# Optimization experiments

Hardware: AMD Instinct MI355X
Metric: run time of the kernel (lower is better)

## Reference

```python
import jax, jax.numpy as jnp
import numpy as np
import math

NUM_HEADS = 4


def setup_inputs() -> dict:
    key = jax.random.key(0)
    k1, k2, k3, k4 = jax.random.split(key, 4)
    b, c, f, t = 8, 512, 32, 64
    x = jax.random.normal(k1, (b, c, f, t), dtype=jnp.float32)
    # Conv1d(k=1) weights stored as 2D (out, in); fan-in scaled like torch default
    qkv_w = jax.random.normal(k2, (3 * c, c), dtype=jnp.float32) / math.sqrt(c)
    qkv_b = jax.random.normal(k3, (3 * c,), dtype=jnp.float32) * 0.02
    proj_w = jax.random.normal(k4, (c, c), dtype=jnp.float32) / math.sqrt(c)
    proj_b = jnp.zeros((c,), dtype=jnp.float32)
    return {"x": x, "qkv_w": qkv_w, "qkv_b": qkv_b, "proj_w": proj_w, "proj_b": proj_b}


def reference(x, qkv_w, qkv_b, proj_w, proj_b):
    b, c, f, t = x.shape
    T = f * t
    xr = x.reshape(b, c, T)  # [b, c, T]
    # Note: original forward computes PositionalEncoding2D(x) but discards it.
    qkv = jnp.einsum('oc,bct->bot', qkv_w, xr) + qkv_b[None, :, None]  # [b, 3c, T]
    H = NUM_HEADS
    ch = c // H
    q, k, v = jnp.split(qkv, 3, axis=1)  # each [b, c, T]
    q = q.reshape(b * H, ch, T)
    k = k.reshape(b * H, ch, T)
    v = v.reshape(b * H, ch, T)
    scale = 1.0 / math.sqrt(math.sqrt(ch))
    w = jnp.einsum('bct,bcs->bts', q * scale, k * scale)  # [b*H, T, T]
    w = jax.nn.softmax(w.astype(jnp.float32), axis=-1).astype(q.dtype)
    a = jnp.einsum('bts,bcs->bct', w, v).reshape(b, c, T)
    h = jnp.einsum('oc,bct->bot', proj_w, a) + proj_b[None, :, None]
    return (xr + h).reshape(b, c, f, t)
```

## Files before the change

kernel.cpp:

```cpp
#include <hip/hip_runtime.h>

#define DEV static __device__ __forceinline__

typedef __attribute__((ext_vector_type(8))) short short8;
typedef __attribute__((ext_vector_type(4))) float f32x4;
typedef __attribute__((ext_vector_type(16))) float f32x16;
typedef __attribute__((ext_vector_type(2))) unsigned int uint2v;

DEV unsigned short f2bf(float f) {
    union { float f; unsigned int u; } v; v.f = f;
    unsigned int u = v.u;
    unsigned int r = (u + 0x7fffu + ((u >> 16) & 1u)) >> 16;
    return (unsigned short)r;
}

DEV unsigned int cvtpk(float lo, float hi) {
    unsigned int r;
    asm("v_cvt_pk_bf16_f32 %0, %1, %2" : "=v"(r) : "v"(lo), "v"(hi));
    return r;
}

DEV float vexp2(float x) {
    float r;
    asm("v_exp_f32 %0, %1" : "=v"(r) : "v"(x));
    return r;
}

DEV float pl32_max(float v) {
    union { float f; unsigned u; } c; c.f = v;
    uint2v r = __builtin_amdgcn_permlane32_swap(c.u, c.u, false, false);
    union { unsigned u; float f; } a, b; a.u = r[0]; b.u = r[1];
    return fmaxf(a.f, b.f);
}
DEV float pl32_sum(float v) {
    union { float f; unsigned u; } c; c.f = v;
    uint2v r = __builtin_amdgcn_permlane32_swap(c.u, c.u, false, false);
    union { unsigned u; float f; } a, b; a.u = r[0]; b.u = r[1];
    return a.f + b.f;
}

DEV unsigned short* swp(unsigned short* base, int row, int col, int rs) {
    int a = ((row * rs + col) << 1) ^ ((row & 7) << 4);
    return (unsigned short*)((char*)base + a);
}

DEV void lds_barrier() {
    asm volatile("s_waitcnt lgkmcnt(0)" ::: "memory");
    __builtin_amdgcn_s_barrier();
}

DEV void gload16(const void* g, void* l) {
    __builtin_amdgcn_global_load_lds((const __attribute__((address_space(1))) void*)g,
                                     (__attribute__((address_space(3))) void*)l, 16, 0, 0);
}

__global__ void prep_kernel(const float* __restrict__ qkv_w,
                            const float* __restrict__ proj_w,
                            unsigned short* __restrict__ Wq,
                            unsigned short* __restrict__ Wp) {
    int i = blockIdx.x * blockDim.x + threadIdx.x;
    int stride = gridDim.x * blockDim.x;
    for (int j = i; j < 1536 * 512; j += stride) Wq[j] = f2bf(qkv_w[j]);
    for (int j = i; j < 512 * 512;  j += stride) Wp[j] = f2bf(proj_w[j]);
}

__global__ __launch_bounds__(256) void transpose_kernel(const float* __restrict__ x,
                                                        unsigned short* __restrict__ Xt) {
    __shared__ unsigned char lt[64 * 128];
    int b  = blockIdx.z;
    int c0 = blockIdx.y * 64;
    int t0 = blockIdx.x * 64;
    int tid = threadIdx.x;
    int tx = tid & 15, cy0 = tid >> 4;
    for (int p = 0; p < 4; ++p) {
        int cy = cy0 + p * 16;
        const float* src = &x[((size_t)(b * 512 + c0 + cy)) * 2048 + t0 + tx * 4];
        f32x4 v = *(const f32x4*)src;
        unsigned long long pk = (unsigned long long)f2bf(v[0])
                              | ((unsigned long long)f2bf(v[1]) << 16)
                              | ((unsigned long long)f2bf(v[2]) << 32)
                              | ((unsigned long long)f2bf(v[3]) << 48);
        int addr = (cy * 128 + tx * 8) ^ ((cy & 7) << 4);
        *(unsigned long long*)(lt + addr) = pk;
    }
    __syncthreads();
    int c16 = (tid & 3) * 16, tr = tid >> 2;
    unsigned short buf[16];
    for (int i = 0; i < 16; ++i) {
        int c = c16 + i;
        int addr = (c * 128 + tr * 2) ^ ((c & 7) << 4);
        buf[i] = *(unsigned short*)(lt + addr);
    }
    unsigned short* dst = &Xt[((size_t)(b * 2048 + t0 + tr)) * 512 + c0 + c16];
    *(short8*)dst       = *(short8*)&buf[0];
    *(short8*)(dst + 8) = *(short8*)&buf[8];
}

template <int ORIENT>
__global__ __launch_bounds__(256, 2) void gemm_qkv_kernel(
    const unsigned short* __restrict__ Wq,
    const unsigned short* __restrict__ Xt,
    const float* __restrict__ qkv_b,
    unsigned short* __restrict__ Qw,
    unsigned short* __restrict__ Kw,
    unsigned short* __restrict__ Vw) {
    __shared__ unsigned short As[2][128 * 64];
    __shared__ unsigned short Bs[2][128 * 64];
    int b  = blockIdx.z;
    int ot = (ORIENT == 0) ? blockIdx.y : (8 + blockIdx.y);
    int o0 = ot * 128, t0 = blockIdx.x * 128;
    int tid = threadIdx.x, lane = tid & 63, w = tid >> 6;
    int lr = lane >> 4, lc = lane & 15;
    int wr = (w >> 1) * 64, wc = (w & 1) * 64;
    f32x4 acc[4][4];
    for (int m = 0; m < 4; m++)
        for (int n = 0; n < 4; n++) acc[m][n] = (f32x4){0.f, 0.f, 0.f, 0.f};

    int r8 = lane >> 3, ck = lane & 7;
    int sc8 = (ck ^ r8) * 8;

    const unsigned short* Wbase = &Wq[(size_t)o0 * 512];
    const unsigned short* Xbase = &Xt[((size_t)(b * 2048) + t0) * 512];

    #define QKV_STAGE(buf, ks)                                                        \
        _Pragma("unroll")                                                             \
        for (int p = 0; p < 4; p++) {                                                 \
            int rowblk = (w * 4 + p) * 8;                                             \
            gload16(&Wbase[(size_t)(rowblk + r8) * 512 + (ks) * 64 + sc8],            \
                    &As[buf][rowblk * 64]);                                           \
            gload16(&Xbase[(size_t)(rowblk + r8) * 512 + (ks) * 64 + sc8],            \
                    &Bs[buf][rowblk * 64]);                                           \
        }

    QKV_STAGE(0, 0);
    asm volatile("s_waitcnt vmcnt(0)" ::: "memory");
    __builtin_amdgcn_s_barrier();
    for (int t = 0; t < 8; ++t) {
        int cur = t & 1;
        if (t < 7) { QKV_STAGE(cur ^ 1, t + 1); }
        unsigned short* Ab = (unsigned short*)As[cur];
        unsigned short* Bb = (unsigned short*)Bs[cur];
        #pragma unroll
        for (int kk = 0; kk < 64; kk += 32) {
            int kb = kk + lr * 8;
            short8 af[4], bfv[4];
            if (ORIENT == 0) {
                for (int m = 0; m < 4; m++) af[m]  = *(const short8*)swp(Bb, wr + m * 16 + lc, kb, 64);
                for (int n = 0; n < 4; n++) bfv[n] = *(const short8*)swp(Ab, wc + n * 16 + lc, kb, 64);
            } else {
                for (int m = 0; m < 4; m++) af[m]  = *(const short8*)swp(Ab, wr + m * 16 + lc, kb, 64);
                for (int n = 0; n < 4; n++) bfv[n] = *(const short8*)swp(Bb, wc + n * 16 + lc, kb, 64);
            }
            for (int m = 0; m < 4; m++)
                for (int n = 0; n < 4; n++)
                    acc[m][n] = __builtin_amdgcn_mfma_f32_16x16x32_bf16(af[m], bfv[n], acc[m][n], 0, 0, 0);
        }
        asm volatile("s_waitcnt vmcnt(0)" ::: "memory");
        __builtin_amdgcn_s_barrier();
    }
    const float scale_k = 0.29730177875068026f;
    const float scale_q = 0.42891498953885586f;
    for (int m = 0; m < 4; m++)
        for (int n = 0; n < 4; n++)
            for (int r = 0; r < 4; r++) {
                int row = wr + m * 16 + lr * 4 + r;
                int col = wc + n * 16 + lc;
                float val = acc[m][n][r];
                if (ORIENT == 0) {
                    int t = t0 + row;
                    int o = o0 + col;
                    float sc = (o < 512) ? scale_q : scale_k;
                    val = (val + qkv_b[o]) * sc;
                    if (o < 512) {
                        int h = o >> 7, cc = o & 127;
                        Qw[((size_t)((b * 4 + h) * 2048 + t)) * 128 + cc] = f2bf(val);
                    } else {
                        int oo = o - 512;
                        int h = oo >> 7, cc = oo & 127;
                        Kw[((size_t)((b * 4 + h) * 2048 + t)) * 128 + cc] = f2bf(val);
                    }
                } else {
                    int o = o0 + row;
                    int t = t0 + col;
                    val += qkv_b[o];
                    int oo = o - 1024;
                    int h = oo >> 7, cc = oo & 127;
                    Vw[((size_t)((b * 4 + h) * 128 + cc)) * 2048 + t] = f2bf(val);
                }
            }
}

__global__ __launch_bounds__(256, 2) void attn_kernel(
    const unsigned short* __restrict__ Qw,
    const unsigned short* __restrict__ Kw,
    const unsigned short* __restrict__ Vw,
    unsigned short* __restrict__ Aw) {
    __shared__ unsigned short lds[32768];
    int bid = blockIdx.x;
    int bh = bid & 31;
    int t0 = (bid >> 5) * 128;
    int tid = threadIdx.x, lane = tid & 63, w = tid >> 6;
    int l31 = lane & 31, hi = lane >> 5;
    int qrow = w * 32;

    const unsigned short* Kbase = &Kw[(size_t)bh * 2048 * 128];
    const unsigned short* Vbase = &Vw[(size_t)bh * 128 * 2048];

    short8 qf[8];
    #pragma unroll
    for (int st = 0; st < 8; st++)
        qf[st] = *(const short8*)&Qw[((size_t)bh * 2048 + t0 + qrow + l31) * 128 + st * 16 + hi * 8];

    f32x16 oacc[4];
    #pragma unroll
    for (int ct = 0; ct < 4; ct++)
        #pragma unroll
        for (int i = 0; i < 16; i++) oacc[ct][i] = 0.f;
    float mst = -1e30f, lst = 0.f;

    int kr = tid >> 4, ko = (tid & 15) * 8;
    int vr = tid >> 3, vo = (tid & 7) * 8;

    short8 kreg[4], vreg[4];
    #pragma unroll
    for (int p = 0; p < 4; p++)
        kreg[p] = *(const short8*)&Kbase[(size_t)(kr + p * 16) * 128 + ko];
    #pragma unroll
    for (int p = 0; p < 4; p++)
        vreg[p] = *(const short8*)&Vbase[(size_t)(vr + p * 32) * 2048 + vo];

    for (int it = 0; it < 32; ++it) {
        int cur = it & 1;
        unsigned short* Kb = lds + cur * 8192;
        unsigned short* Vb = lds + 16384 + cur * 8192;
        #pragma unroll
        for (int p = 0; p < 4; p++) *(short8*)swp(Kb, kr + p * 16, ko, 128) = kreg[p];
        #pragma unroll
        for (int p = 0; p < 4; p++) *(short8*)swp(Vb, vr + p * 32, vo, 64) = vreg[p];
        if (it + 1 < 32) {
            int s1 = (it + 1) * 64;
            #pragma unroll
            for (int p = 0; p < 4; p++)
                kreg[p] = *(const short8*)&Kbase[(size_t)(s1 + kr + p * 16) * 128 + ko];
            #pragma unroll
            for (int p = 0; p < 4; p++)
                vreg[p] = *(const short8*)&Vbase[(size_t)(vr + p * 32) * 2048 + s1 + vo];
        }
        lds_barrier();

        f32x16 s0, s1v;
        #pragma unroll
        for (int i = 0; i < 16; i++) { s0[i] = 0.f; s1v[i] = 0.f; }
        __builtin_amdgcn_s_setprio(1);
        #pragma unroll
        for (int st = 0; st < 8; st++) {
            short8 k0 = *(const short8*)swp(Kb, l31,      st * 16 + hi * 8, 128);
            short8 k1 = *(const short8*)swp(Kb, 32 + l31, st * 16 + hi * 8, 128);
            s0  = __builtin_amdgcn_mfma_f32_32x32x16_bf16(k0, qf[st], s0, 0, 0, 0);
            s1v = __builtin_amdgcn_mfma_f32_32x32x16_bf16(k1, qf[st], s1v, 0, 0, 0);
        }
        __builtin_amdgcn_s_setprio(0);

        float m16[16];
        #pragma unroll
        for (int i = 0; i < 16; i++) m16[i] = fmaxf(s0[i], s1v[i]);
        #pragma unroll
        for (int sdt = 8; sdt > 0; sdt >>= 1)
            #pragma unroll
            for (int i = 0; i < 8; i++)
                if (i < sdt) m16[i] = fmaxf(m16[i], m16[i + sdt]);
        float mx = pl32_max(m16[0]);
        if (!__all(mx <= mst + 11.541560327111707f)) {
            float mnew = fmaxf(mst, mx);
            float resc = vexp2(mst - mnew);
            mst = mnew;
            lst *= resc;
            #pragma unroll
            for (int ct = 0; ct < 4; ct++)
                #pragma unroll
                for (int i = 0; i < 16; i++) oacc[ct][i] *= resc;
        }
        float pe[32];
        #pragma unroll
        for (int i = 0; i < 16; i++) pe[i]      = vexp2(s0[i]  - mst);
        #pragma unroll
        for (int i = 0; i < 16; i++) pe[16 + i] = vexp2(s1v[i] - mst);
        float a16[16];
        #pragma unroll
        for (int i = 0; i < 16; i++) a16[i] = pe[i] + pe[16 + i];
        #pragma unroll
        for (int sdt = 8; sdt > 0; sdt >>= 1)
            #pragma unroll
            for (int i = 0; i < 8; i++)
                if (i < sdt) a16[i] = a16[i] + a16[i + sdt];
        lst += pl32_sum(a16[0]);

        short8 pf[4];
        #pragma unroll
        for (int st = 0; st < 4; st++) {
            unsigned X0 = cvtpk(pe[st * 8 + 0], pe[st * 8 + 1]);
            unsigned X1 = cvtpk(pe[st * 8 + 2], pe[st * 8 + 3]);
            unsigned Y0 = cvtpk(pe[st * 8 + 4], pe[st * 8 + 5]);
            unsigned Y1 = cvtpk(pe[st * 8 + 6], pe[st * 8 + 7]);
            uint2v r0 = __builtin_amdgcn_permlane32_swap(X0, Y0, false, false);
            uint2v r1 = __builtin_amdgcn_permlane32_swap(X1, Y1, false, false);
            union { unsigned u[4]; short8 s; } uu;
            uu.u[0] = r0[0];
            uu.u[1] = r1[0];
            uu.u[2] = r0[1];
            uu.u[3] = r1[1];
            pf[st] = uu.s;
        }

        __builtin_amdgcn_s_setprio(1);
        #pragma unroll
        for (int ct = 0; ct < 4; ct++)
            #pragma unroll
            for (int st = 0; st < 4; st++) {
                short8 va = *(const short8*)swp(Vb, ct * 32 + l31, st * 16 + hi * 8, 64);
                oacc[ct] = __builtin_amdgcn_mfma_f32_32x32x16_bf16(va, pf[st], oacc[ct], 0, 0, 0);
            }
        __builtin_amdgcn_s_setprio(0);
    }

    __syncthreads();
    unsigned short* ep = lds + w * 4096;
    float invl = 1.f / lst;
    #pragma unroll
    for (int ct = 0; ct < 4; ct++)
        #pragma unroll
        for (int i = 0; i < 8; i++) {
            int c = (2 * i & 3) + 8 * (i >> 1) + 4 * hi + 32 * ct;
            unsigned d = cvtpk(oacc[ct][2 * i] * invl, oacc[ct][2 * i + 1] * invl);
            *(unsigned*)swp(ep, l31, c, 128) = d;
        }
    asm volatile("" ::: "memory");
    int q = lane >> 1, hf = lane & 1;
    int b = bh >> 2, h = bh & 3;
    #pragma unroll
    for (int p = 0; p < 8; p++) {
        short8 v = *(const short8*)swp(ep, q, hf * 64 + p * 8, 128);
        *(short8*)&Aw[((size_t)(b * 2048) + t0 + qrow + q) * 512 + h * 128 + hf * 64 + p * 8] = v;
    }
}

#define LP 72
__global__ __launch_bounds__(256, 2) void gemm_proj_kernel(
    const unsigned short* __restrict__ Wp,
    const unsigned short* __restrict__ Aw,
    const float* __restrict__ proj_b,
    const float* __restrict__ x,
    float* __restrict__ out) {
    __shared__ unsigned short Ws[2][128][LP];
    __shared__ unsigned short Bs[2][128][LP];
    int b  = blockIdx.z;
    int o0 = blockIdx.y * 128, t0 = blockIdx.x * 128;
    int tid = threadIdx.x, lane = tid & 63, w = tid >> 6;
    int lr = lane >> 4, lc = lane & 15;
    int wr = (w >> 1) * 64, wc = (w & 1) * 64;
    f32x4 acc[4][4];
    for (int m = 0; m < 4; m++)
        for (int n = 0; n < 4; n++) acc[m][n] = (f32x4){0.f, 0.f, 0.f, 0.f};
    int srow = tid >> 3, soff = (tid & 7) * 8;

    short8 wreg[4], breg[4];
    #pragma unroll
    for (int p = 0; p < 4; p++) {
        wreg[p] = *(const short8*)&Wp[(size_t)(o0 + srow + p * 32) * 512 + soff];
        breg[p] = *(const short8*)&Aw[((size_t)(b * 2048) + t0 + srow + p * 32) * 512 + soff];
    }
    for (int t = 0; t < 8; ++t) {
        int cur = t & 1;
        #pragma unroll
        for (int p = 0; p < 4; p++) {
            *(short8*)&Ws[cur][srow + p * 32][soff] = wreg[p];
            *(short8*)&Bs[cur][srow + p * 32][soff] = breg[p];
        }
        if (t < 7) {
            int k1 = (t + 1) * 64;
            #pragma unroll
            for (int p = 0; p < 4; p++) {
                wreg[p] = *(const short8*)&Wp[(size_t)(o0 + srow + p * 32) * 512 + k1 + soff];
                breg[p] = *(const short8*)&Aw[((size_t)(b * 2048) + t0 + srow + p * 32) * 512 + k1 + soff];
            }
        }
        lds_barrier();
        for (int kk = 0; kk < 64; kk += 32) {
            int kb = kk + lr * 8;
            short8 af[4], bfv[4];
            for (int m = 0; m < 4; m++) af[m]  = *(const short8*)&Ws[cur][wr + m * 16 + lc][kb];
            for (int n = 0; n < 4; n++) bfv[n] = *(const short8*)&Bs[cur][wc + n * 16 + lc][kb];
            for (int m = 0; m < 4; m++)
                for (int n = 0; n < 4; n++)
                    acc[m][n] = __builtin_amdgcn_mfma_f32_16x16x32_bf16(af[m], bfv[n], acc[m][n], 0, 0, 0);
        }
        __builtin_amdgcn_s_barrier();
    }
    for (int m = 0; m < 4; m++)
        for (int n = 0; n < 4; n++)
            for (int r = 0; r < 4; r++) {
                int o = o0 + wr + m * 16 + lr * 4 + r;
                int t = t0 + wc + n * 16 + lc;
                size_t idx = ((size_t)(b * 512) + o) * 2048 + t;
                out[idx] = x[idx] + acc[m][n][r] + proj_b[o];
            }
}

extern "C" void kernel_launch(void* const* d_in, const int* in_sizes, int n_in,
                              void* d_out, int out_size, void* d_ws, size_t ws_size,
                              hipStream_t stream) {
    const float* x      = (const float*)d_in[0];
    const float* qkv_w  = (const float*)d_in[1];
    const float* qkv_b  = (const float*)d_in[2];
    const float* proj_w = (const float*)d_in[3];
    const float* proj_b = (const float*)d_in[4];
    float* out = (float*)d_out;

    unsigned short* ws = (unsigned short*)d_ws;
    unsigned short* Wq = ws;
    unsigned short* Wp = Wq + (size_t)1536 * 512;
    unsigned short* Xt = Wp + (size_t)512 * 512;
    unsigned short* Qw = Xt + (size_t)8 * 2048 * 512;
    unsigned short* Kw = Qw + (size_t)32 * 2048 * 128;
    unsigned short* Vw = Kw + (size_t)32 * 2048 * 128;
    unsigned short* Aw = Vw + (size_t)32 * 2048 * 128;

    prep_kernel<<<dim3(512), dim3(256), 0, stream>>>(qkv_w, proj_w, Wq, Wp);
    transpose_kernel<<<dim3(32, 8, 8), dim3(256), 0, stream>>>(x, Xt);
    gemm_qkv_kernel<0><<<dim3(16, 8, 8), dim3(256), 0, stream>>>(Wq, Xt, qkv_b, Qw, Kw, Vw);
    gemm_qkv_kernel<1><<<dim3(16, 4, 8), dim3(256), 0, stream>>>(Wq, Xt, qkv_b, Qw, Kw, Vw);
    attn_kernel<<<dim3(512), dim3(256), 0, stream>>>(Qw, Kw, Vw, Aw);
    gemm_proj_kernel<<<dim3(16, 4, 8), dim3(256), 0, stream>>>(Wp, Aw, proj_b, x, out);
}
```

Measured before the change: 165.3 us.

## Split attention KV range into two halves with async LDS loads and combine pass

The attention kernel now gives each wave 64 query rows (two 32-row blocks), so every K/V tile read from LDS feeds twice as many MFMAs. The key range is split into two halves processed by separate blocks, which keeps the grid at 512 blocks. Each half writes a partial output plus its running max and sum, and a new combine kernel merges them into the final attention output. K/V staging moves from register round-trips to direct global-to-LDS loads. The cost is an extra kernel launch, extra global traffic for the bf16 partials, and higher register pressure.

```diff
diff --git a/kernel.cpp b/kernel.cpp
--- a/kernel.cpp
+++ b/kernel.cpp
@@ -13,6 +13,10 @@
     unsigned int r = (u + 0x7fffu + ((u >> 16) & 1u)) >> 16;
     return (unsigned short)r;
 }
+DEV float bf2f(unsigned short s) {
+    union { unsigned int u; float f; } v; v.u = ((unsigned int)s) << 16;
+    return v.f;
+}
 
 DEV unsigned int cvtpk(float lo, float hi) {
     unsigned int r;
@@ -52,6 +56,22 @@
 DEV void gload16(const void* g, void* l) {
     __builtin_amdgcn_global_load_lds((const __attribute__((address_space(1))) void*)g,
                                      (__attribute__((address_space(3))) void*)l, 16, 0, 0);
+}
+
+DEV short8 mk_pf(float v0, float v1, float v2, float v3,
+                 float v4, float v5, float v6, float v7) {
+    unsigned X0 = cvtpk(v0, v1);
+    unsigned X1 = cvtpk(v2, v3);
+    unsigned Y0 = cvtpk(v4, v5);
+    unsigned Y1 = cvtpk(v6, v7);
+    uint2v r0 = __builtin_amdgcn_permlane32_swap(X0, Y0, false, false);
+    uint2v r1 = __builtin_amdgcn_permlane32_swap(X1, Y1, false, false);
+    union { unsigned u[4]; short8 s; } uu;
+    uu.u[0] = r0[0];
+    uu.u[1] = r1[0];
+    uu.u[2] = r0[1];
+    uu.u[3] = r1[1];
+    return uu.s;
 }
 
 __global__ void prep_kernel(const float* __restrict__ qkv_w,
@@ -194,122 +214,117 @@
     const unsigned short* __restrict__ Qw,
     const unsigned short* __restrict__ Kw,
     const unsigned short* __restrict__ Vw,
-    unsigned short* __restrict__ Aw) {
+    unsigned short* __restrict__ Op,
+    float* __restrict__ Ml) {
     __shared__ unsigned short lds[32768];
     int bid = blockIdx.x;
     int bh = bid & 31;
-    int t0 = (bid >> 5) * 128;
+    int rest = bid >> 5;
+    int t0 = (rest & 7) * 256;
+    int side = rest >> 3;
+    int sbase = side * 1024;
     int tid = threadIdx.x, lane = tid & 63, w = tid >> 6;
     int l31 = lane & 31, hi = lane >> 5;
-    int qrow = w * 32;
+    int qrow = w * 64;
 
     const unsigned short* Kbase = &Kw[(size_t)bh * 2048 * 128];
     const unsigned short* Vbase = &Vw[(size_t)bh * 128 * 2048];
 
-    short8 qf[8];
+    short8 qf[2][8];
     #pragma unroll
-    for (int st = 0; st < 8; st++)
-        qf[st] = *(const short8*)&Qw[((size_t)bh * 2048 + t0 + qrow + l31) * 128 + st * 16 + hi * 8];
-
-    f32x16 oacc[4];
+    for (int qb = 0; qb < 2; qb++)
+        #pragma unroll
+        for (int st = 0; st < 8; st++)
+            qf[qb][st] = *(const short8*)&Qw[((size_t)bh * 2048 + t0 + qrow + qb * 32 + l31) * 128 + st * 16 + hi * 8];
+
+    f32x16 oacc[2][4];
     #pragma unroll
-    for (int ct = 0; ct < 4; ct++)
-        #pragma unroll
-        for (int i = 0; i < 16; i++) oacc[ct][i] = 0.f;
-    float mst = -1e30f, lst = 0.f;
-
-    int kr = tid >> 4, ko = (tid & 15) * 8;
-    int vr = tid >> 3, vo = (tid & 7) * 8;
-
-    short8 kreg[4], vreg[4];
-    #pragma unroll
-    for (int p = 0; p < 4; p++)
-        kreg[p] = *(const short8*)&Kbase[(size_t)(kr + p * 16) * 128 + ko];
-    #pragma unroll
-    for (int p = 0; p < 4; p++)
-        vreg[p] = *(const short8*)&Vbase[(size_t)(vr + p * 32) * 2048 + vo];
-
-    for (int it = 0; it < 32; ++it) {
+    for (int qb = 0; qb < 2; qb++)
+        #pragma unroll
+        for (int ct = 0; ct < 4; ct++)
+            #pragma unroll
+            for (int i = 0; i < 16; i++) oacc[qb][ct][i] = 0.f;
+    float mst[2] = {-1e30f, -1e30f}, lst[2] = {0.f, 0.f};
+
+    int krow = tid >> 4, kck = tid & 15;
+    int vrow = tid >> 3, vck = tid & 7;
+    int kswz = (kck ^ (krow & 7)) * 8;
+    int vswz = (vck ^ (vrow & 7)) * 8;
+
+    #define A_STAGE(buf, s0_)                                                          \
+        _Pragma("unroll")                                                              \
+        for (int p = 0; p < 4; p++)                                                    \
+            gload16(&Kbase[(size_t)((s0_) + krow + p * 16) * 128 + kswz],              \
+                    (char*)lds + (buf) * 16384 + w * 1024 + p * 4096);                 \
+        _Pragma("unroll")                                                              \
+        for (int p = 0; p < 4; p++)                                                    \
+            gload16(&Vbase[(size_t)(vrow + p * 32) * 2048 + (s0_) + vswz],             \
+                    (char*)lds + 32768 + (buf) * 16384 + w * 1024 + p * 4096);
+
+    A_STAGE(0, sbase);
+    asm volatile("s_waitcnt vmcnt(0)" ::: "memory");
+    __builtin_amdgcn_s_barrier();
+
+    for (int it = 0; it < 16; ++it) {
         int cur = it & 1;
+        if (it + 1 < 16) { A_STAGE(cur ^ 1, sbase + (it + 1) * 64); }
         unsigned short* Kb = lds + cur * 8192;
         unsigned short* Vb = lds + 16384 + cur * 8192;
-        #pragma unroll
-        for (int p = 0; p < 4; p++) *(short8*)swp(Kb, kr + p * 16, ko, 128) = kreg[p];
-        #pragma unroll
-        for (int p = 0; p < 4; p++) *(short8*)swp(Vb, vr + p * 32, vo, 64) = vreg[p];
-        if (it + 1 < 32) {
-            int s1 = (it + 1) * 64;
-            #pragma unroll
-            for (int p = 0; p < 4; p++)
-                kreg[p] = *(const short8*)&Kbase[(size_t)(s1 + kr + p * 16) * 128 + ko];
-            #pragma unroll
-            for (int p = 0; p < 4; p++)
-                vreg[p] = *(const short8*)&Vbase[(size_t)(vr + p * 32) * 2048 + s1 + vo];
-        }
-        lds_barrier();
-
-        f32x16 s0, s1v;
-        #pragma unroll
-        for (int i = 0; i < 16; i++) { s0[i] = 0.f; s1v[i] = 0.f; }
-        __builtin_amdgcn_s_setprio(1);
-        #pragma unroll
-        for (int st = 0; st < 8; st++) {
-            short8 k0 = *(const short8*)swp(Kb, l31,      st * 16 + hi * 8, 128);
-            short8 k1 = *(const short8*)swp(Kb, 32 + l31, st * 16 + hi * 8, 128);
-            s0  = __builtin_amdgcn_mfma_f32_32x32x16_bf16(k0, qf[st], s0, 0, 0, 0);
-            s1v = __builtin_amdgcn_mfma_f32_32x32x16_bf16(k1, qf[st], s1v, 0, 0, 0);
-        }
-        __builtin_amdgcn_s_setprio(0);
-
-        float m16[16];
-        #pragma unroll
-        for (int i = 0; i < 16; i++) m16[i] = fmaxf(s0[i], s1v[i]);
-        #pragma unroll
-        for (int sdt = 8; sdt > 0; sdt >>= 1)
+
+        short8 pf[2][4];
+        #pragma unroll
+        for (int qb = 0; qb < 2; qb++) {
+            f32x16 sA, sB;
+            #pragma unroll
+            for (int i = 0; i < 16; i++) { sA[i] = 0.f; sB[i] = 0.f; }
+            __builtin_amdgcn_s_setprio(1);
+            #pragma unroll
+            for (int st = 0; st < 8; st++) {
+                short8 k0 = *(const short8*)swp(Kb, l31,      st * 16 + hi * 8, 128);
+                short8 k1 = *(const short8*)swp(Kb, 32 + l31, st * 16 + hi * 8, 128);
+                sA = __builtin_amdgcn_mfma_f32_32x32x16_bf16(k0, qf[qb][st], sA, 0, 0, 0);
+                sB = __builtin_amdgcn_mfma_f32_32x32x16_bf16(k1, qf[qb][st], sB, 0, 0, 0);
+            }
+            __builtin_amdgcn_s_setprio(0);
+
+            float m8[8];
             #pragma unroll
             for (int i = 0; i < 8; i++)
-                if (i < sdt) m16[i] = fmaxf(m16[i], m16[i + sdt]);
-        float mx = pl32_max(m16[0]);
-        if (!__all(mx <= mst + 11.541560327111707f)) {
-            float mnew = fmaxf(mst, mx);
-            float resc = vexp2(mst - mnew);
-            mst = mnew;
-            lst *= resc;
-            #pragma unroll
-            for (int ct = 0; ct < 4; ct++)
+                m8[i] = fmaxf(fmaxf(sA[i], sA[i + 8]), fmaxf(sB[i], sB[i + 8]));
+            #pragma unroll
+            for (int sdt = 4; sdt > 0; sdt >>= 1)
                 #pragma unroll
-                for (int i = 0; i < 16; i++) oacc[ct][i] *= resc;
-        }
-        float pe[32];
-        #pragma unroll
-        for (int i = 0; i < 16; i++) pe[i]      = vexp2(s0[i]  - mst);
-        #pragma unroll
-        for (int i = 0; i < 16; i++) pe[16 + i] = vexp2(s1v[i] - mst);
-        float a16[16];
-        #pragma unroll
-        for (int i = 0; i < 16; i++) a16[i] = pe[i] + pe[16 + i];
-        #pragma unroll
-        for (int sdt = 8; sdt > 0; sdt >>= 1)
-            #pragma unroll
-            for (int i = 0; i < 8; i++)
-                if (i < sdt) a16[i] = a16[i] + a16[i + sdt];
-        lst += pl32_sum(a16[0]);
-
-        short8 pf[4];
-        #pragma unroll
-        for (int st = 0; st < 4; st++) {
-            unsigned X0 = cvtpk(pe[st * 8 + 0], pe[st * 8 + 1]);
-            unsigned X1 = cvtpk(pe[st * 8 + 2], pe[st * 8 + 3]);
-            unsigned Y0 = cvtpk(pe[st * 8 + 4], pe[st * 8 + 5]);
-            unsigned Y1 = cvtpk(pe[st * 8 + 6], pe[st * 8 + 7]);
-            uint2v r0 = __builtin_amdgcn_permlane32_swap(X0, Y0, false, false);
-            uint2v r1 = __builtin_amdgcn_permlane32_swap(X1, Y1, false, false);
-            union { unsigned u[4]; short8 s; } uu;
-            uu.u[0] = r0[0];
-            uu.u[1] = r1[0];
-            uu.u[2] = r0[1];
-            uu.u[3] = r1[1];
-            pf[st] = uu.s;
+                for (int i = 0; i < 4; i++)
+                    if (i < sdt) m8[i] = fmaxf(m8[i], m8[i + sdt]);
+            float mx = pl32_max(m8[0]);
+            if (!__all(mx <= mst[qb] + 11.541560327111707f)) {
+                float mnew = fmaxf(mst[qb], mx);
+                float resc = vexp2(mst[qb] - mnew);
+                mst[qb] = mnew;
+                lst[qb] *= resc;
+                #pragma unroll
+                for (int ct = 0; ct < 4; ct++)
+                    #pragma unroll
+                    for (int i = 0; i < 16; i++) oacc[qb][ct][i] *= resc;
+            }
+            #pragma unroll
+            for (int i = 0; i < 16; i++) sA[i] = vexp2(sA[i] - mst[qb]);
+            #pragma unroll
+            for (int i = 0; i < 16; i++) sB[i] = vexp2(sB[i] - mst[qb]);
+            float a8[8];
+            #pragma unroll
+            for (int i = 0; i < 8; i++) a8[i] = (sA[i] + sA[i + 8]) + (sB[i] + sB[i + 8]);
+            #pragma unroll
+            for (int sdt = 4; sdt > 0; sdt >>= 1)
+                #pragma unroll
+                for (int i = 0; i < 4; i++)
+                    if (i < sdt) a8[i] = a8[i] + a8[i + sdt];
+            lst[qb] += pl32_sum(a8[0]);
+
+            pf[qb][0] = mk_pf(sA[0], sA[1], sA[2], sA[3], sA[4], sA[5], sA[6], sA[7]);
+            pf[qb][1] = mk_pf(sA[8], sA[9], sA[10], sA[11], sA[12], sA[13], sA[14], sA[15]);
+            pf[qb][2] = mk_pf(sB[0], sB[1], sB[2], sB[3], sB[4], sB[5], sB[6], sB[7]);
+            pf[qb][3] = mk_pf(sB[8], sB[9], sB[10], sB[11], sB[12], sB[13], sB[14], sB[15]);
         }
 
         __builtin_amdgcn_s_setprio(1);
@@ -318,30 +333,71 @@
             #pragma unroll
             for (int st = 0; st < 4; st++) {
                 short8 va = *(const short8*)swp(Vb, ct * 32 + l31, st * 16 + hi * 8, 64);
-                oacc[ct] = __builtin_amdgcn_mfma_f32_32x32x16_bf16(va, pf[st], oacc[ct], 0, 0, 0);
+                oacc[0][ct] = __builtin_amdgcn_mfma_f32_32x32x16_bf16(va, pf[0][st], oacc[0][ct], 0, 0, 0);
+                oacc[1][ct] = __builtin_amdgcn_mfma_f32_32x32x16_bf16(va, pf[1][st], oacc[1][ct], 0, 0, 0);
             }
         __builtin_amdgcn_s_setprio(0);
+        asm volatile("s_waitcnt vmcnt(0)" ::: "memory");
+        __builtin_amdgcn_s_barrier();
     }
 
     __syncthreads();
     unsigned short* ep = lds + w * 4096;
-    float invl = 1.f / lst;
+    int q = lane >> 1, hf = lane & 1;
+    unsigned short* Opb = Op + (((size_t)side * 32 + bh) * 2048) * 128;
+    float* Mlb = Ml + (((size_t)side * 32 + bh) * 2048) * 2;
     #pragma unroll
-    for (int ct = 0; ct < 4; ct++)
-        #pragma unroll
-        for (int i = 0; i < 8; i++) {
-            int c = (2 * i & 3) + 8 * (i >> 1) + 4 * hi + 32 * ct;
-            unsigned d = cvtpk(oacc[ct][2 * i] * invl, oacc[ct][2 * i + 1] * invl);
-            *(unsigned*)swp(ep, l31, c, 128) = d;
-        }
-    asm volatile("" ::: "memory");
-    int q = lane >> 1, hf = lane & 1;
-    int b = bh >> 2, h = bh & 3;
+    for (int qb = 0; qb < 2; qb++) {
+        float invl = 1.f / lst[qb];
+        #pragma unroll
+        for (int ct = 0; ct < 4; ct++)
+            #pragma unroll
+            for (int i = 0; i < 8; i++) {
+                int c = (2 * i & 3) + 8 * (i >> 1) + 4 * hi + 32 * ct;
+                unsigned d = cvtpk(oacc[qb][ct][2 * i] * invl, oacc[qb][ct][2 * i + 1] * invl);
+                *(unsigned*)swp(ep, l31, c, 128) = d;
+            }
+        asm volatile("" ::: "memory");
+        int trow = t0 + qrow + qb * 32;
+        #pragma unroll
+        for (int p = 0; p < 8; p++) {
+            short8 v = *(const short8*)swp(ep, q, hf * 64 + p * 8, 128);
+            *(short8*)&Opb[(size_t)(trow + q) * 128 + hf * 64 + p * 8] = v;
+        }
+        if (hi == 0) {
+            Mlb[(size_t)(trow + l31) * 2 + 0] = mst[qb];
+            Mlb[(size_t)(trow + l31) * 2 + 1] = lst[qb];
+        }
+        asm volatile("" ::: "memory");
+    }
+}
+
+__global__ __launch_bounds__(256) void combine_kernel(
+    const unsigned short* __restrict__ Op,
+    const float* __restrict__ Ml,
+    unsigned short* __restrict__ Aw) {
+    int g = blockIdx.x * 256 + threadIdx.x;
+    int c8 = g & 15;
+    int row = g >> 4;
+    int bh = row >> 11;
+    int t  = row & 2047;
+    const size_t SIDE = (size_t)32 * 2048 * 128;
+    size_t o0 = (size_t)row * 128 + c8 * 8;
+    float m0 = Ml[(size_t)row * 2], l0 = Ml[(size_t)row * 2 + 1];
+    float m1 = Ml[((size_t)32 * 2048 + row) * 2], l1 = Ml[((size_t)32 * 2048 + row) * 2 + 1];
+    float M = fmaxf(m0, m1);
+    float w0 = vexp2(m0 - M) * l0;
+    float w1 = vexp2(m1 - M) * l1;
+    float inv = 1.f / (w0 + w1);
+    w0 *= inv; w1 *= inv;
+    short8 a = *(const short8*)&Op[o0];
+    short8 b = *(const short8*)&Op[SIDE + o0];
+    unsigned short outv[8];
     #pragma unroll
-    for (int p = 0; p < 8; p++) {
-        short8 v = *(const short8*)swp(ep, q, hf * 64 + p * 8, 128);
-        *(short8*)&Aw[((size_t)(b * 2048) + t0 + qrow + q) * 512 + h * 128 + hf * 64 + p * 8] = v;
-    }
+    for (int j = 0; j < 8; j++)
+        outv[j] = f2bf(bf2f((unsigned short)a[j]) * w0 + bf2f((unsigned short)b[j]) * w1);
+    int bq = bh >> 2, h = bh & 3;
+    *(short8*)&Aw[((size_t)(bq * 2048) + t) * 512 + h * 128 + c8 * 8] = *(short8*)outv;
 }
 
 #define LP 72
@@ -424,11 +480,14 @@
     unsigned short* Kw = Qw + (size_t)32 * 2048 * 128;
     unsigned short* Vw = Kw + (size_t)32 * 2048 * 128;
     unsigned short* Aw = Vw + (size_t)32 * 2048 * 128;
+    unsigned short* Opp = Aw + (size_t)8 * 2048 * 512;
+    float* Ml = (float*)(Opp + (size_t)2 * 32 * 2048 * 128);
 
     prep_kernel<<<dim3(512), dim3(256), 0, stream>>>(qkv_w, proj_w, Wq, Wp);
     transpose_kernel<<<dim3(32, 8, 8), dim3(256), 0, stream>>>(x, Xt);
     gemm_qkv_kernel<0><<<dim3(16, 8, 8), dim3(256), 0, stream>>>(Wq, Xt, qkv_b, Qw, Kw, Vw);
     gemm_qkv_kernel<1><<<dim3(16, 4, 8), dim3(256), 0, stream>>>(Wq, Xt, qkv_b, Qw, Kw, Vw);
-    attn_kernel<<<dim3(512), dim3(256), 0, stream>>>(Qw, Kw, Vw, Aw);
+    attn_kernel<<<dim3(512), dim3(256), 0, stream>>>(Qw, Kw, Vw, Opp, Ml);
+    combine_kernel<<<dim3(4096), dim3(256), 0, stream>>>(Opp, Ml, Aw);
     gemm_proj_kernel<<<dim3(16, 4, 8), dim3(256), 0, stream>>>(Wp, Aw, proj_b, x, out);
 }
```

Result: slower. 264.3 us (+59.8%).

## Stage K/V tiles with direct global-to-LDS loads in double-buffered pipeline

Applied to the files above, without the earlier changes.

The register-staged prefetch of K and V tiles is replaced by direct global-to-LDS loads (gload16) into the next buffer, issued at the top of each iteration. The XOR swizzle moves into the global source address, and the loop ends with a vmcnt wait plus a barrier. This is meant to cut VGPR pressure and the LDS store instructions, and to overlap loads with the MFMA work. It relies on gload16's per-wave layout matching the swp read pattern, and the end-of-loop full wait may serialize part of the load.

```diff
diff --git a/kernel.cpp b/kernel.cpp
--- a/kernel.cpp
+++ b/kernel.cpp
@@ -218,35 +218,30 @@
         for (int i = 0; i < 16; i++) oacc[ct][i] = 0.f;
     float mst = -1e30f, lst = 0.f;
 
-    int kr = tid >> 4, ko = (tid & 15) * 8;
-    int vr = tid >> 3, vo = (tid & 7) * 8;
-
-    short8 kreg[4], vreg[4];
-    #pragma unroll
-    for (int p = 0; p < 4; p++)
-        kreg[p] = *(const short8*)&Kbase[(size_t)(kr + p * 16) * 128 + ko];
-    #pragma unroll
-    for (int p = 0; p < 4; p++)
-        vreg[p] = *(const short8*)&Vbase[(size_t)(vr + p * 32) * 2048 + vo];
+    int krow = tid >> 4, kck = tid & 15;
+    int vrow = tid >> 3, vck = tid & 7;
+    int kswz = (kck ^ (krow & 7)) * 8;
+    int vswz = (vck ^ (vrow & 7)) * 8;
+
+    #define A_STAGE(buf, s0_)                                                          \
+        _Pragma("unroll")                                                              \
+        for (int p = 0; p < 4; p++)                                                    \
+            gload16(&Kbase[(size_t)((s0_) + krow + p * 16) * 128 + kswz],              \
+                    (char*)lds + (buf) * 16384 + w * 1024 + p * 4096);                 \
+        _Pragma("unroll")                                                              \
+        for (int p = 0; p < 4; p++)                                                    \
+            gload16(&Vbase[(size_t)(vrow + p * 32) * 2048 + (s0_) + vswz],             \
+                    (char*)lds + 32768 + (buf) * 16384 + w * 1024 + p * 4096);
+
+    A_STAGE(0, 0);
+    asm volatile("s_waitcnt vmcnt(0)" ::: "memory");
+    __builtin_amdgcn_s_barrier();
 
     for (int it = 0; it < 32; ++it) {
         int cur = it & 1;
+        if (it + 1 < 32) { A_STAGE(cur ^ 1, (it + 1) * 64); }
         unsigned short* Kb = lds + cur * 8192;
         unsigned short* Vb = lds + 16384 + cur * 8192;
-        #pragma unroll
-        for (int p = 0; p < 4; p++) *(short8*)swp(Kb, kr + p * 16, ko, 128) = kreg[p];
-        #pragma unroll
-        for (int p = 0; p < 4; p++) *(short8*)swp(Vb, vr + p * 32, vo, 64) = vreg[p];
-        if (it + 1 < 32) {
-            int s1 = (it + 1) * 64;
-            #pragma unroll
-            for (int p = 0; p < 4; p++)
-                kreg[p] = *(const short8*)&Kbase[(size_t)(s1 + kr + p * 16) * 128 + ko];
-            #pragma unroll
-            for (int p = 0; p < 4; p++)
-                vreg[p] = *(const short8*)&Vbase[(size_t)(vr + p * 32) * 2048 + s1 + vo];
-        }
-        lds_barrier();
 
         f32x16 s0, s1v;
         #pragma unroll
@@ -321,6 +316,8 @@
                 oacc[ct] = __builtin_amdgcn_mfma_f32_32x32x16_bf16(va, pf[st], oacc[ct], 0, 0, 0);
             }
         __builtin_amdgcn_s_setprio(0);
+        asm volatile("s_waitcnt vmcnt(0)" ::: "memory");
+        __builtin_amdgcn_s_barrier();
     }
 
     __syncthreads();
```

After: 166.5 us. Within noise of the previous version (+0.7%).
